# Optimization experiments

Measured on AMD Instinct MI355X. Metric: run time of the kernel, lower is better.

## Reference

```python
import jax, jax.numpy as jnp
import numpy as np

BN_EPS = 1e-5

def _bn(x, gamma, beta, relu=True):
    # training-mode BatchNorm over all dims except channel (last)
    axes = tuple(range(x.ndim - 1))
    mu = jnp.mean(x, axes, keepdims=True)
    var = jnp.var(x, axes, keepdims=True)
    y = (x - mu) / jnp.sqrt(var + BN_EPS) * gamma + beta
    return jax.nn.relu(y) if relu else y

def _l2norm(x, eps):
    # F.normalize: x / max(||x||, eps)
    n = jnp.sqrt(jnp.sum(x * x, axis=-1, keepdims=True))
    return x / jnp.maximum(n, eps)

def setup_inputs() -> dict:
    key = jax.random.key(0)
    ks = jax.random.split(key, 16)
    B, N, H, W, C = 2, 512, 16, 32, 64
    IN_DIM = 10 + C + C + 2  # 140
    MLP3 = [128, 64]
    s = 0.02
    inp = {
        "warped_xyz": jax.random.normal(ks[0], (B, N, 3), jnp.float32),
        "warped_points": jax.random.normal(ks[1], (B, N, C), jnp.float32),
        "RF3": jax.random.normal(ks[2], (B, C, H, W), jnp.float32),
        "RF3_index": jax.random.normal(ks[3], (B, 3, H, W), jnp.float32),
        "lidar_z": jax.random.uniform(ks[4], (B, N, 1), jnp.float32),
        # conv1x1 stack (mlp3)
        "W1": jax.random.normal(ks[5], (IN_DIM, MLP3[0]), jnp.float32) * s,
        "b1": jnp.zeros((MLP3[0],), jnp.float32),
        "g1": jnp.ones((MLP3[0],), jnp.float32),
        "be1": jnp.zeros((MLP3[0],), jnp.float32),
        "W2": jax.random.normal(ks[6], (MLP3[0], MLP3[1]), jnp.float32) * s,
        "b2": jnp.zeros((MLP3[1],), jnp.float32),
        "g2": jnp.ones((MLP3[1],), jnp.float32),
        "be2": jnp.zeros((MLP3[1],), jnp.float32),
        # conv1d stack (mlp4 = [feats_dim//2], then 2 logits)
        "M1w": jax.random.normal(ks[7], (MLP3[1], MLP3[1] // 2), jnp.float32) * s,
        "M1b": jnp.zeros((MLP3[1] // 2,), jnp.float32),
        "M1g": jnp.ones((MLP3[1] // 2,), jnp.float32),
        "M1be": jnp.zeros((MLP3[1] // 2,), jnp.float32),
        "M2w": jax.random.normal(ks[8], (MLP3[1] // 2, 2), jnp.float32) * s,
        "M2b": jnp.zeros((2,), jnp.float32),
    }
    return inp

def reference(warped_xyz, warped_points, RF3, RF3_index, lidar_z,
              W1, b1, g1, be1, W2, b2, g2, be2,
              M1w, M1b, M1g, M1be, M2w, M2b):
    B, N, _ = warped_xyz.shape
    _, Ci, H, W_ = RF3.shape
    M = H * W_
    RF3_bnc = RF3.transpose(0, 2, 3, 1).reshape(B, M, Ci)          # [B,M,C]
    idx_bnc = RF3_index.transpose(0, 2, 3, 1).reshape(B, M, 3)     # [B,M,3]

    src_xyz = warped_xyz[:, :, None, :]                             # [B,N,1,3]
    dst_xyz = idx_bnc[:, None, :, :]                                # [B,1,M,3]
    euc = (src_xyz - dst_xyz)[..., :2]                              # [B,N,M,2]
    euc_norm = jnp.sqrt(euc[..., 0:1] ** 2 + euc[..., 1:2] ** 2)    # [B,N,M,1]

    xyz_z = (warped_xyz * lidar_z)[:, :, None, :]                   # [B,N,1,3]
    src_pts = warped_points[:, :, None, :]                          # [B,N,1,C]
    dst_pts = RF3_bnc[:, None, :, :]                                # [B,1,M,C]

    geom = jnp.concatenate([
        jnp.broadcast_to(xyz_z, (B, N, M, 3)),
        jnp.broadcast_to(src_pts[..., :2], (B, N, M, 2)),
        jnp.broadcast_to(dst_xyz[..., :2], (B, N, M, 2)),
        euc, euc_norm], axis=-1)                                    # [B,N,M,10]
    desc = jnp.concatenate([
        jnp.broadcast_to(src_pts, (B, N, M, Ci)),
        jnp.broadcast_to(dst_pts, (B, N, M, Ci))], axis=-1)         # [B,N,M,2C]

    # cal_sim: cosine sim between lidar feats (src) and image feats (dst)
    src_n = _l2norm(warped_points, 1e-12)
    dst_n = _l2norm(RF3_bnc, 1e-12)
    cos = jnp.einsum('bnc,bmc->bnm', src_n, dst_n)                  # [B,N,M]
    s1 = cos / (jnp.max(cos, axis=2, keepdims=True) + 1e-6)         # src->dst norm
    s2 = cos / (jnp.max(cos, axis=1, keepdims=True) + 1e-10)        # dst->src norm
    sim = jnp.stack([s1, s2], axis=-1)                              # [B,N,M,2]

    feats = jnp.concatenate([geom, desc, sim], axis=-1)             # [B,N,M,140]
    feats = _bn(jnp.einsum('bnmi,io->bnmo', feats, W1) + b1, g1, be1)
    feats = _bn(jnp.einsum('bnmi,io->bnmo', feats, W2) + b2, g2, be2)

    aw = jax.nn.softmax(jnp.max(feats, axis=-1), axis=-1)           # [B,N,M]
    att = jnp.einsum('bnm,bnmc->bnc', aw, feats)                    # [B,N,C]

    att = _bn(att @ M1w + M1b, M1g, M1be)
    logits = att @ M2w + M2b                                        # [B,N,2]
    return logits
```

## Files before the change

### kernel.cpp

```cpp
#include <hip/hip_runtime.h>
#include <hip/hip_bf16.h>

#define B_ 2
#define N_ 512
#define M_ 512
#define C_ 64
#define O1 128
#define O2 64
#define O3 32
#define PBIG 524288.0f
#define P3   1024.0f

typedef short s8v __attribute__((ext_vector_type(8)));
typedef float f4v __attribute__((ext_vector_type(4)));

#define WS_SRCN 0
#define WS_DSTN 65536
#define WS_U    131072
#define WS_V    262144
#define WS_DXY  393216
#define WS_COS  395264
#define WS_RMAX 919552
#define WS_CMAX 920576
#define WS_ST1  921600
#define WS_ST2  925696
#define WS_ST3  927744
#define WS_Z    928768
#define WS_X2   961536

__device__ __forceinline__ unsigned fenc(float f){
  unsigned b = __float_as_uint(f);
  return (b & 0x80000000u) ? ~b : (b | 0x80000000u);
}
__device__ __forceinline__ float fdec(unsigned u){
  unsigned b = (u & 0x80000000u) ? (u & 0x7fffffffu) : ~u;
  return __uint_as_float(b);
}
__device__ __forceinline__ unsigned short f2bf(float f){
  unsigned u = __float_as_uint(f);
  unsigned r = (u + 0x7fffu + ((u >> 16) & 1u)) >> 16;
  return (unsigned short)r;
}
__device__ __forceinline__ float bf2f(unsigned short h){
  return __uint_as_float(((unsigned)h) << 16);
}

__global__ __launch_bounds__(128) void k1a(const float* __restrict__ wxyz,
    const float* __restrict__ wpts, const float* __restrict__ lz,
    const float* __restrict__ W1, float* __restrict__ ws){
  int blk = blockIdx.x; int b = blk >> 9, n = blk & 511; int t = threadIdx.x;
  int bn = b*N_ + n;
  __shared__ float wp[64]; __shared__ float sxyz[3]; __shared__ float slz; __shared__ float srn;
  if (t < 64) wp[t] = wpts[bn*64 + t];
  if (t >= 64 && t < 67) sxyz[t-64] = wxyz[bn*3 + (t-64)];
  if (t == 67) slz = lz[bn];
  __syncthreads();
  if (t < 64){
    float v = wp[t]*wp[t];
    v += __shfl_down(v,32); v += __shfl_down(v,16); v += __shfl_down(v,8);
    v += __shfl_down(v,4);  v += __shfl_down(v,2);  v += __shfl_down(v,1);
    if (t == 0) srn = 1.0f / fmaxf(sqrtf(v), 1e-12f);
  }
  __syncthreads();
  if (t < 64) ws[WS_SRCN + bn*64 + t] = wp[t]*srn;
  int o = t;
  float x = sxyz[0], y = sxyz[1], z = sxyz[2], l = slz;
  float acc = x*l*W1[0*O1+o] + y*l*W1[1*O1+o] + z*l*W1[2*O1+o]
            + wp[0]*W1[3*O1+o] + wp[1]*W1[4*O1+o]
            + x*W1[7*O1+o] + y*W1[8*O1+o];
  #pragma unroll 8
  for (int c = 0; c < 64; ++c) acc += wp[c]*W1[(10+c)*O1+o];
  ws[WS_U + bn*O1 + o] = acc;
}

__global__ __launch_bounds__(128) void k1b(const float* __restrict__ rf3,
    const float* __restrict__ rf3i, const float* __restrict__ W1, float* __restrict__ ws){
  int blk = blockIdx.x; int b = blk >> 9, m = blk & 511; int t = threadIdx.x;
  int bm = b*M_ + m;
  __shared__ float rf[64]; __shared__ float sdx, sdy, srn;
  if (t < 64) rf[t] = rf3[(b*64 + t)*512 + m];
  if (t == 64) sdx = rf3i[(b*3 + 0)*512 + m];
  if (t == 65) sdy = rf3i[(b*3 + 1)*512 + m];
  __syncthreads();
  if (t < 64){
    float v = rf[t]*rf[t];
    v += __shfl_down(v,32); v += __shfl_down(v,16); v += __shfl_down(v,8);
    v += __shfl_down(v,4);  v += __shfl_down(v,2);  v += __shfl_down(v,1);
    if (t == 0) srn = 1.0f / fmaxf(sqrtf(v), 1e-12f);
  }
  __syncthreads();
  if (t < 64) ws[WS_DSTN + bm*64 + t] = rf[t]*srn;
  if (t == 0){ ws[WS_DXY + bm*2+0] = sdx; ws[WS_DXY + bm*2+1] = sdy; }
  int o = t;
  float acc = sdx*(W1[5*O1+o] - W1[7*O1+o]) + sdy*(W1[6*O1+o] - W1[8*O1+o]);
  #pragma unroll 8
  for (int c = 0; c < 64; ++c) acc += rf[c]*W1[(74+c)*O1+o];
  ws[WS_V + bm*O1 + o] = acc;
}

__global__ __launch_bounds__(256) void k2(float* __restrict__ ws){
  int blk = blockIdx.x; int b = blk >> 9, n = blk & 511; int t = threadIdx.x;
  int bn = b*N_ + n;
  __shared__ __align__(16) float sn[64];
  __shared__ float dnt[64*65];
  __shared__ float part[4*64];
  if (t < 64) sn[t] = ws[WS_SRCN + bn*64 + t];
  unsigned* cmax = (unsigned*)ws + WS_CMAX;
  float lmax = -1e30f;
  for (int chunk = 0; chunk < 8; ++chunk){
    __syncthreads();
    const float4* src = (const float4*)(ws + WS_DSTN + (size_t)(b*M_ + chunk*64)*64);
    #pragma unroll
    for (int i = 0; i < 4; ++i){
      float4 v = src[t + i*256];
      int base = (t + i*256)*4; int mm = base >> 6, c = base & 63;
      float* dp = &dnt[mm*65 + c];
      dp[0]=v.x; dp[1]=v.y; dp[2]=v.z; dp[3]=v.w;
    }
    __syncthreads();
    {
      int mm = t & 63, cg = t >> 6;
      const float* dr = &dnt[mm*65 + cg*16];
      const float* sr = &sn[cg*16];
      float p = 0.f;
      #pragma unroll
      for (int k = 0; k < 16; ++k) p += sr[k]*dr[k];
      part[cg*64 + mm] = p;
    }
    __syncthreads();
    if (t < 64){
      float d = part[t] + part[64+t] + part[128+t] + part[192+t];
      int m = chunk*64 + t;
      ws[WS_COS + bn*M_ + m] = d;
      atomicMax(&cmax[b*M_ + m], fenc(d));
      lmax = fmaxf(lmax, d);
    }
  }
  if (t < 64){
    lmax = fmaxf(lmax, __shfl_xor(lmax,32)); lmax = fmaxf(lmax, __shfl_xor(lmax,16));
    lmax = fmaxf(lmax, __shfl_xor(lmax,8));  lmax = fmaxf(lmax, __shfl_xor(lmax,4));
    lmax = fmaxf(lmax, __shfl_xor(lmax,2));  lmax = fmaxf(lmax, __shfl_xor(lmax,1));
    if (t == 0) ws[WS_RMAX + bn] = lmax;
  }
}

__global__ __launch_bounds__(128) void k3(const float* __restrict__ wxyz,
    const float* __restrict__ W1, const float* __restrict__ b1, float* __restrict__ ws){
  int blk = blockIdx.x; int b = blk >> 9, n = blk & 511; int t = threadIdx.x;
  int bn = b*N_ + n;
  __shared__ float s_en[512], s_s1[512], s_s2[512];
  __shared__ float sx, sy, srm;
  if (t == 0){ sx = wxyz[bn*3+0]; sy = wxyz[bn*3+1]; srm = ws[WS_RMAX+bn]; }
  __syncthreads();
  const unsigned* cmax = (const unsigned*)ws + WS_CMAX;
  #pragma unroll
  for (int i = 0; i < 4; ++i){
    int m = t + i*128;
    float dx = ws[WS_DXY + (b*M_+m)*2+0], dy = ws[WS_DXY + (b*M_+m)*2+1];
    float ex = sx-dx, ey = sy-dy;
    s_en[m] = sqrtf(ex*ex + ey*ey);
    float cv = ws[WS_COS + bn*M_ + m];
    s_s1[m] = cv/(srm + 1e-6f);
    s_s2[m] = cv/(fdec(cmax[b*M_+m]) + 1e-10f);
  }
  __syncthreads();
  int o = t;
  float u  = ws[WS_U + bn*O1 + o] + b1[o];
  float w9 = W1[9*O1+o], wa = W1[138*O1+o], wb = W1[139*O1+o];
  float sum = 0.f, ssq = 0.f;
  const float* Vp = ws + WS_V + b*M_*O1 + o;
  #pragma unroll 8
  for (int m = 0; m < 512; ++m){
    float xv = u + Vp[m*O1] + s_en[m]*w9 + s_s1[m]*wa + s_s2[m]*wb;
    sum += xv; ssq += xv*xv;
  }
  int rep = blk & 15;
  atomicAdd(&ws[WS_ST1 + rep*256 + o], sum);
  atomicAdd(&ws[WS_ST1 + rep*256 + 128 + o], ssq);
}

#define HROW 136
__global__ __launch_bounds__(256) void k4(const float* __restrict__ wxyz,
    const float* __restrict__ W1, const float* __restrict__ b1,
    const float* __restrict__ g1, const float* __restrict__ be1,
    const float* __restrict__ W2, float* __restrict__ ws){
  int blk = blockIdx.x;
  int b = blk >> 11; int rem = blk & 2047; int n = rem >> 2; int mc = rem & 3;
  int t = threadIdx.x; int bn = b*N_ + n; int m0 = mc*128;
  __shared__ unsigned short hA[128*HROW];
  __shared__ unsigned short wB[64*HROW];
  __shared__ float s_en[128], s_s1[128], s_s2[128];
  __shared__ float sP0[128], sA1[128], sW9[128], sWa[128], sWb[128];
  __shared__ float ls[64], lq[64];
  __shared__ float sx, sy, srm;
  if (t == 128) sx = wxyz[bn*3+0];
  if (t == 129) sy = wxyz[bn*3+1];
  if (t == 130) srm = ws[WS_RMAX+bn];
  if (t < 64){ ls[t] = 0.f; lq[t] = 0.f; }
  if (t < 128){
    int o = t; float s = 0.f, q = 0.f;
    #pragma unroll
    for (int r = 0; r < 16; ++r){ s += ws[WS_ST1 + r*256 + o]; q += ws[WS_ST1 + r*256 + 128 + o]; }
    float mu = s/PBIG; float var = q/PBIG - mu*mu;
    float istd = rsqrtf(var + 1e-5f);
    float A1 = g1[o]*istd; float C1 = be1[o] - mu*A1;
    float u = ws[WS_U + bn*O1 + o] + b1[o];
    sP0[o] = u*A1 + C1; sA1[o] = A1;
    sW9[o] = W1[9*O1+o]*A1; sWa[o] = W1[138*O1+o]*A1; sWb[o] = W1[139*O1+o]*A1;
  }
  for (int idx = t; idx < 8192; idx += 256){
    int o = idx >> 6, c = idx & 63;
    wB[c*HROW + o] = f2bf(W2[idx]);
  }
  __syncthreads();
  if (t < 128){
    int m = m0 + t;
    float dx = ws[WS_DXY + (b*M_+m)*2+0], dy = ws[WS_DXY + (b*M_+m)*2+1];
    float ex = sx-dx, ey = sy-dy;
    s_en[t] = sqrtf(ex*ex + ey*ey);
    float cv = ws[WS_COS + bn*M_ + m];
    s_s1[t] = cv/(srm + 1e-6f);
    s_s2[t] = cv/(fdec(((const unsigned*)ws)[WS_CMAX + b*M_+m]) + 1e-10f);
  }
  __syncthreads();
  {
    int lane = t & 63, g = t >> 6;
    const float* Vb = ws + WS_V + (size_t)(b*M_ + m0)*O1;
    int o0 = 2*lane;
    #pragma unroll 8
    for (int i = 0; i < 32; ++i){
      int ml = g + 4*i;
      float en = s_en[ml], s1 = s_s1[ml], s2 = s_s2[ml];
      float2 v = *(const float2*)(Vb + ml*O1 + o0);
      float h0 = fmaxf(sP0[o0]   + v.x*sA1[o0]   + en*sW9[o0]   + s1*sWa[o0]   + s2*sWb[o0],   0.f);
      float h1 = fmaxf(sP0[o0+1] + v.y*sA1[o0+1] + en*sW9[o0+1] + s1*sWa[o0+1] + s2*sWb[o0+1], 0.f);
      unsigned pack = (unsigned)f2bf(h0) | ((unsigned)f2bf(h1) << 16);
      *(unsigned*)&hA[ml*HROW + o0] = pack;
    }
  }
  __syncthreads();
  int lane = t & 63, w = t >> 6;
  int l16 = lane & 15, quad = lane >> 4;
  f4v acc[2][4];
  #pragma unroll
  for (int i = 0; i < 2; ++i)
    #pragma unroll
    for (int j = 0; j < 4; ++j) acc[i][j] = (f4v){0.f,0.f,0.f,0.f};
  int ar0 = (w*32 + l16)*HROW, ar1 = (w*32 + 16 + l16)*HROW;
  #pragma unroll
  for (int k0 = 0; k0 < 128; k0 += 32){
    int ko = k0 + quad*8;
    s8v a0 = *(const s8v*)&hA[ar0 + ko];
    s8v a1 = *(const s8v*)&hA[ar1 + ko];
    #pragma unroll
    for (int ct = 0; ct < 4; ++ct){
      s8v bb = *(const s8v*)&wB[(ct*16 + l16)*HROW + ko];
      acc[0][ct] = __builtin_amdgcn_mfma_f32_16x16x32_bf16(a0, bb, acc[0][ct], 0,0,0);
      acc[1][ct] = __builtin_amdgcn_mfma_f32_16x16x32_bf16(a1, bb, acc[1][ct], 0,0,0);
    }
  }
  unsigned short* x2p = (unsigned short*)(ws + WS_X2);
  size_t xbase = (size_t)bn*M_*O2;
  #pragma unroll
  for (int ct = 0; ct < 4; ++ct){
    int c = ct*16 + l16;
    float s = 0.f, q = 0.f;
    #pragma unroll
    for (int mt = 0; mt < 2; ++mt){
      #pragma unroll
      for (int r = 0; r < 4; ++r){
        float v = acc[mt][ct][r];
        int m = m0 + w*32 + mt*16 + quad*4 + r;
        x2p[xbase + (size_t)m*O2 + c] = f2bf(v);
        s += v; q += v*v;
      }
    }
    s += __shfl_xor(s,16); s += __shfl_xor(s,32);
    q += __shfl_xor(q,16); q += __shfl_xor(q,32);
    if (quad == 0){ atomicAdd(&ls[c], s); atomicAdd(&lq[c], q); }
  }
  __syncthreads();
  int rep = blk & 15;
  if (t < 64) atomicAdd(&ws[WS_ST2 + rep*128 + t], ls[t]);
  else if (t < 128) atomicAdd(&ws[WS_ST2 + rep*128 + t], lq[t-64]);
}

__global__ __launch_bounds__(256) void k5(const float* __restrict__ g2,
    const float* __restrict__ be2, const float* __restrict__ M1w,
    const float* __restrict__ M1b, float* __restrict__ ws){
  int blk = blockIdx.x; int b = blk >> 9, n = blk & 511; int t = threadIdx.x;
  int bn = b*N_ + n;
  __shared__ float sa2[64], sc2[64];
  __shared__ float s_mx[512];
  __shared__ float s_aw[512];
  __shared__ float red[256];
  __shared__ float part[32*64];
  __shared__ float s_att[64];
  __shared__ float sgmax, sinvS;
  if (t < 64){
    float s = 0.f, q = 0.f;
    #pragma unroll
    for (int r = 0; r < 16; ++r){ s += ws[WS_ST2 + r*128 + t]; q += ws[WS_ST2 + r*128 + 64 + t]; }
    float mu = s/PBIG, var = q/PBIG - mu*mu;
    float istd = rsqrtf(var + 1e-5f);
    float A2 = g2[t]*istd;
    sa2[t] = A2; sc2[t] = be2[t] - mu*A2;
  }
  __syncthreads();
  int j8 = t & 7, r32 = t >> 3;
  int c0 = j8*8;
  float a2r[8], c2r[8];
  #pragma unroll
  for (int j = 0; j < 8; ++j){ a2r[j] = sa2[c0+j]; c2r[j] = sc2[c0+j]; }
  const unsigned short* xp = (const unsigned short*)(ws + WS_X2) + (size_t)bn*M_*O2;
  s8v xv[16];
  #pragma unroll
  for (int s = 0; s < 16; ++s)
    xv[s] = *(const s8v*)(xp + (size_t)(s*32 + r32)*64 + c0);
  #pragma unroll
  for (int s = 0; s < 16; ++s){
    float mx = 0.f;
    #pragma unroll
    for (int j = 0; j < 8; ++j){
      float x = bf2f((unsigned short)xv[s][j]);
      float y = fmaxf(a2r[j]*x + c2r[j], 0.f);
      mx = fmaxf(mx, y);
    }
    mx = fmaxf(mx, __shfl_xor(mx,1));
    mx = fmaxf(mx, __shfl_xor(mx,2));
    mx = fmaxf(mx, __shfl_xor(mx,4));
    if (j8 == 0) s_mx[s*32 + r32] = mx;
  }
  __syncthreads();
  red[t] = fmaxf(s_mx[t], s_mx[t+256]);
  __syncthreads();
  for (int s = 128; s > 0; s >>= 1){ if (t < s) red[t] = fmaxf(red[t], red[t+s]); __syncthreads(); }
  if (t == 0) sgmax = red[0];
  __syncthreads();
  float e0 = expf(s_mx[t] - sgmax), e1 = expf(s_mx[t+256] - sgmax);
  s_aw[t] = e0; s_aw[t+256] = e1;
  red[t] = e0 + e1;
  __syncthreads();
  for (int s = 128; s > 0; s >>= 1){ if (t < s) red[t] += red[t+s]; __syncthreads(); }
  if (t == 0) sinvS = 1.0f / red[0];
  __syncthreads();
  float acc[8];
  #pragma unroll
  for (int j = 0; j < 8; ++j) acc[j] = 0.f;
  #pragma unroll
  for (int s = 0; s < 16; ++s){
    float aw = s_aw[s*32 + r32];
    #pragma unroll
    for (int j = 0; j < 8; ++j){
      float x = bf2f((unsigned short)xv[s][j]);
      float y = fmaxf(a2r[j]*x + c2r[j], 0.f);
      acc[j] += aw*y;
    }
  }
  #pragma unroll
  for (int j = 0; j < 8; ++j) part[r32*64 + c0 + j] = acc[j];
  __syncthreads();
  if (t < 64){
    float a = 0.f;
    #pragma unroll 8
    for (int r = 0; r < 32; ++r) a += part[r*64 + t];
    s_att[t] = a * sinvS;
  }
  __syncthreads();
  if (t < 32){
    float z = M1b[t];
    #pragma unroll 8
    for (int c = 0; c < 64; ++c) z += s_att[c]*M1w[c*32 + t];
    ws[WS_Z + bn*32 + t] = z;
    int rep = blk & 15;
    atomicAdd(&ws[WS_ST3 + rep*64 + t], z);
    atomicAdd(&ws[WS_ST3 + rep*64 + 32 + t], z*z);
  }
}

__global__ __launch_bounds__(256) void k6(const float* __restrict__ M1g,
    const float* __restrict__ M1be, const float* __restrict__ M2w,
    const float* __restrict__ M2b, const float* __restrict__ ws, float* __restrict__ out){
  int t = threadIdx.x; int s = blockIdx.x*256 + t;
  __shared__ float sa3[32], sc3[32];
  if (t < 32){
    float su = 0.f, q = 0.f;
    #pragma unroll
    for (int r = 0; r < 16; ++r){ su += ws[WS_ST3 + r*64 + t]; q += ws[WS_ST3 + r*64 + 32 + t]; }
    float mu = su/P3, var = q/P3 - mu*mu;
    float istd = rsqrtf(var + 1e-5f);
    float A3 = M1g[t]*istd;
    sa3[t] = A3; sc3[t] = M1be[t] - mu*A3;
  }
  __syncthreads();
  float a0 = M2b[0], a1 = M2b[1];
  #pragma unroll
  for (int j = 0; j < 32; ++j){
    float y = fmaxf(ws[WS_Z + s*32 + j]*sa3[j] + sc3[j], 0.f);
    a0 += y*M2w[j*2+0]; a1 += y*M2w[j*2+1];
  }
  out[s*2+0] = a0; out[s*2+1] = a1;
}

extern "C" void kernel_launch(void* const* d_in, const int* in_sizes, int n_in,
                              void* d_out, int out_size, void* d_ws, size_t ws_size,
                              hipStream_t stream){
  const float* wxyz = (const float*)d_in[0];
  const float* wpts = (const float*)d_in[1];
  const float* rf3  = (const float*)d_in[2];
  const float* rf3i = (const float*)d_in[3];
  const float* lz   = (const float*)d_in[4];
  const float* W1   = (const float*)d_in[5];
  const float* b1   = (const float*)d_in[6];
  const float* g1   = (const float*)d_in[7];
  const float* be1  = (const float*)d_in[8];
  const float* W2   = (const float*)d_in[9];
  const float* g2   = (const float*)d_in[11];
  const float* be2  = (const float*)d_in[12];
  const float* M1w  = (const float*)d_in[13];
  const float* M1b  = (const float*)d_in[14];
  const float* M1g  = (const float*)d_in[15];
  const float* M1be = (const float*)d_in[16];
  const float* M2w  = (const float*)d_in[17];
  const float* M2b  = (const float*)d_in[18];
  float* ws  = (float*)d_ws;
  float* out = (float*)d_out;
  hipMemsetAsync(ws + WS_CMAX, 0, (1024 + 4096 + 2048 + 1024)*sizeof(float), stream);
  k1a<<<1024,128,0,stream>>>(wxyz, wpts, lz, W1, ws);
  k1b<<<1024,128,0,stream>>>(rf3, rf3i, W1, ws);
  k2 <<<1024,256,0,stream>>>(ws);
  k3 <<<1024,128,0,stream>>>(wxyz, W1, b1, ws);
  k4 <<<4096,256,0,stream>>>(wxyz, W1, b1, g1, be1, W2, ws);
  k5 <<<1024,256,0,stream>>>(g2, be2, M1w, M1b, ws);
  k6 <<<4,256,0,stream>>>(M1g, M1be, M2w, M2b, ws, out);
}
```

Measured before the change: 247.6 us.

## Precompute BN1 folding and W2 fragments once; build MFMA A operands in registers

A new k3b kernel folds the BN1 scale and shift into per-point P0, pre-scaled V and W9/Wa/Wb vectors, and writes W2 as bf16 in MFMA-fragment order to workspace. k4 no longer recomputes the BN statistics or re-converts W2 in each of its 4096 blocks. It also builds the bf16 A operands directly in registers with truncating packs instead of staging them through shared memory, and it swaps operand order to get coalesced packed stores. k3 is split over 256 threads with half the m range each. Costs are an extra kernel launch plus a pass over V, and bf16 truncation in place of round-to-nearest, which changes numerics slightly.

```diff
diff --git a/kernel.cpp b/kernel.cpp
--- a/kernel.cpp
+++ b/kernel.cpp
@@ -16,6 +16,7 @@
 
 #define WS_SRCN 0
 #define WS_DSTN 65536
+#define WS_P0   0
 #define WS_U    131072
 #define WS_V    262144
 #define WS_DXY  393216
@@ -26,6 +27,8 @@
 #define WS_ST2  925696
 #define WS_ST3  927744
 #define WS_Z    928768
+#define WS_W2F  928768
+#define WS_W9S  932864
 #define WS_X2   961536
 
 __device__ __forceinline__ unsigned fenc(float f){
@@ -43,6 +46,14 @@
 }
 __device__ __forceinline__ float bf2f(unsigned short h){
   return __uint_as_float(((unsigned)h) << 16);
+}
+__device__ __forceinline__ unsigned pk_trunc(float lo, float hi){
+  return __builtin_amdgcn_perm(__float_as_uint(hi), __float_as_uint(lo), 0x07060302u);
+}
+__device__ __forceinline__ f4v relu4(f4v z){
+  z[0] = fmaxf(z[0], 0.f); z[1] = fmaxf(z[1], 0.f);
+  z[2] = fmaxf(z[2], 0.f); z[3] = fmaxf(z[3], 0.f);
+  return z;
 }
 
 __global__ __launch_bounds__(128) void k1a(const float* __restrict__ wxyz,
@@ -144,7 +155,7 @@
   }
 }
 
-__global__ __launch_bounds__(128) void k3(const float* __restrict__ wxyz,
+__global__ __launch_bounds__(256) void k3(const float* __restrict__ wxyz,
     const float* __restrict__ W1, const float* __restrict__ b1, float* __restrict__ ws){
   int blk = blockIdx.x; int b = blk >> 9, n = blk & 511; int t = threadIdx.x;
   int bn = b*N_ + n;
@@ -154,8 +165,8 @@
   __syncthreads();
   const unsigned* cmax = (const unsigned*)ws + WS_CMAX;
   #pragma unroll
-  for (int i = 0; i < 4; ++i){
-    int m = t + i*128;
+  for (int i = 0; i < 2; ++i){
+    int m = t + i*256;
     float dx = ws[WS_DXY + (b*M_+m)*2+0], dy = ws[WS_DXY + (b*M_+m)*2+1];
     float ex = sx-dx, ey = sy-dy;
     s_en[m] = sqrtf(ex*ex + ey*ey);
@@ -164,13 +175,14 @@
     s_s2[m] = cv/(fdec(cmax[b*M_+m]) + 1e-10f);
   }
   __syncthreads();
-  int o = t;
+  int o = t & 127, mh = t >> 7;
   float u  = ws[WS_U + bn*O1 + o] + b1[o];
   float w9 = W1[9*O1+o], wa = W1[138*O1+o], wb = W1[139*O1+o];
   float sum = 0.f, ssq = 0.f;
   const float* Vp = ws + WS_V + b*M_*O1 + o;
+  int mBeg = mh*256, mEnd = mBeg + 256;
   #pragma unroll 8
-  for (int m = 0; m < 512; ++m){
+  for (int m = mBeg; m < mEnd; ++m){
     float xv = u + Vp[m*O1] + s_en[m]*w9 + s_s1[m]*wa + s_s2[m]*wb;
     sum += xv; ssq += xv*xv;
   }
@@ -179,38 +191,60 @@
   atomicAdd(&ws[WS_ST1 + rep*256 + 128 + o], ssq);
 }
 
-#define HROW 136
-__global__ __launch_bounds__(256) void k4(const float* __restrict__ wxyz,
-    const float* __restrict__ W1, const float* __restrict__ b1,
-    const float* __restrict__ g1, const float* __restrict__ be1,
-    const float* __restrict__ W2, float* __restrict__ ws){
+__global__ __launch_bounds__(128) void k3b(const float* __restrict__ W1,
+    const float* __restrict__ b1, const float* __restrict__ g1,
+    const float* __restrict__ be1, const float* __restrict__ W2, float* __restrict__ ws){
+  int blk = blockIdx.x; int t = threadIdx.x;
+  int o = t;
+  float s = 0.f, q = 0.f;
+  #pragma unroll
+  for (int r = 0; r < 16; ++r){ s += ws[WS_ST1 + r*256 + o]; q += ws[WS_ST1 + r*256 + 128 + o]; }
+  float mu = s/PBIG, var = q/PBIG - mu*mu;
+  float istd = rsqrtf(var + 1e-5f);
+  float A1 = g1[o]*istd, C1 = be1[o] - mu*A1;
+  if (blk < 1024){
+    int bn = blk;
+    ws[WS_P0 + bn*O1 + o] = (ws[WS_U + bn*O1 + o] + b1[o])*A1 + C1;
+  } else if (blk < 1040){
+    int r0 = (blk - 1024)*64;
+    for (int r = 0; r < 64; ++r)
+      ws[WS_V + (size_t)(r0 + r)*O1 + o] *= A1;
+  } else {
+    ws[WS_W9S + o]       = W1[9*O1+o]*A1;
+    ws[WS_W9S + 128 + o] = W1[138*O1+o]*A1;
+    ws[WS_W9S + 256 + o] = W1[139*O1+o]*A1;
+    unsigned short* wf = (unsigned short*)(ws + WS_W2F);
+    for (int i = t; i < 8192; i += 128){
+      int j = i & 7, ll = (i >> 3) & 63, ct = (i >> 9) & 3, k0q = i >> 11;
+      int oo = k0q*32 + (ll >> 4)*8 + j, c = ct*16 + (ll & 15);
+      wf[i] = f2bf(W2[oo*O2 + c]);
+    }
+  }
+}
+
+__global__ __launch_bounds__(256, 4) void k4(const float* __restrict__ wxyz,
+    float* __restrict__ ws){
   int blk = blockIdx.x;
   int b = blk >> 11; int rem = blk & 2047; int n = rem >> 2; int mc = rem & 3;
   int t = threadIdx.x; int bn = b*N_ + n; int m0 = mc*128;
-  __shared__ unsigned short hA[128*HROW];
-  __shared__ unsigned short wB[64*HROW];
+  __shared__ __align__(16) unsigned short wBf[8192];
+  __shared__ __align__(16) float p0s[128], w9s[128], was[128], wbs[128];
   __shared__ float s_en[128], s_s1[128], s_s2[128];
-  __shared__ float sP0[128], sA1[128], sW9[128], sWa[128], sWb[128];
   __shared__ float ls[64], lq[64];
   __shared__ float sx, sy, srm;
-  if (t == 128) sx = wxyz[bn*3+0];
-  if (t == 129) sy = wxyz[bn*3+1];
-  if (t == 130) srm = ws[WS_RMAX+bn];
+  if (t == 0){ sx = wxyz[bn*3+0]; sy = wxyz[bn*3+1]; srm = ws[WS_RMAX+bn]; }
   if (t < 64){ ls[t] = 0.f; lq[t] = 0.f; }
+  {
+    const s8v* g = (const s8v*)(ws + WS_W2F);
+    s8v* l = (s8v*)wBf;
+    #pragma unroll
+    for (int c2 = 0; c2 < 4; ++c2) l[c2*256 + t] = g[c2*256 + t];
+  }
   if (t < 128){
-    int o = t; float s = 0.f, q = 0.f;
-    #pragma unroll
-    for (int r = 0; r < 16; ++r){ s += ws[WS_ST1 + r*256 + o]; q += ws[WS_ST1 + r*256 + 128 + o]; }
-    float mu = s/PBIG; float var = q/PBIG - mu*mu;
-    float istd = rsqrtf(var + 1e-5f);
-    float A1 = g1[o]*istd; float C1 = be1[o] - mu*A1;
-    float u = ws[WS_U + bn*O1 + o] + b1[o];
-    sP0[o] = u*A1 + C1; sA1[o] = A1;
-    sW9[o] = W1[9*O1+o]*A1; sWa[o] = W1[138*O1+o]*A1; sWb[o] = W1[139*O1+o]*A1;
-  }
-  for (int idx = t; idx < 8192; idx += 256){
-    int o = idx >> 6, c = idx & 63;
-    wB[c*HROW + o] = f2bf(W2[idx]);
+    p0s[t] = ws[WS_P0 + bn*O1 + t];
+    w9s[t] = ws[WS_W9S + t];
+    was[t] = ws[WS_W9S + 128 + t];
+    wbs[t] = ws[WS_W9S + 256 + t];
   }
   __syncthreads();
   if (t < 128){
@@ -223,61 +257,66 @@
     s_s2[t] = cv/(fdec(((const unsigned*)ws)[WS_CMAX + b*M_+m]) + 1e-10f);
   }
   __syncthreads();
-  {
-    int lane = t & 63, g = t >> 6;
-    const float* Vb = ws + WS_V + (size_t)(b*M_ + m0)*O1;
-    int o0 = 2*lane;
-    #pragma unroll 8
-    for (int i = 0; i < 32; ++i){
-      int ml = g + 4*i;
-      float en = s_en[ml], s1 = s_s1[ml], s2 = s_s2[ml];
-      float2 v = *(const float2*)(Vb + ml*O1 + o0);
-      float h0 = fmaxf(sP0[o0]   + v.x*sA1[o0]   + en*sW9[o0]   + s1*sWa[o0]   + s2*sWb[o0],   0.f);
-      float h1 = fmaxf(sP0[o0+1] + v.y*sA1[o0+1] + en*sW9[o0+1] + s1*sWa[o0+1] + s2*sWb[o0+1], 0.f);
-      unsigned pack = (unsigned)f2bf(h0) | ((unsigned)f2bf(h1) << 16);
-      *(unsigned*)&hA[ml*HROW + o0] = pack;
-    }
-  }
-  __syncthreads();
-  int lane = t & 63, w = t >> 6;
-  int l16 = lane & 15, quad = lane >> 4;
+  int ll = t & 63, w = t >> 6, l16 = ll & 15, quad = ll >> 4;
+  int mb = m0 + w*32;
+  float en0 = s_en[w*32 + l16],     s10 = s_s1[w*32 + l16],     s20 = s_s2[w*32 + l16];
+  float en1 = s_en[w*32 + 16 + l16], s11 = s_s1[w*32 + 16 + l16], s21 = s_s2[w*32 + 16 + l16];
   f4v acc[2][4];
   #pragma unroll
   for (int i = 0; i < 2; ++i)
     #pragma unroll
     for (int j = 0; j < 4; ++j) acc[i][j] = (f4v){0.f,0.f,0.f,0.f};
-  int ar0 = (w*32 + l16)*HROW, ar1 = (w*32 + 16 + l16)*HROW;
-  #pragma unroll
-  for (int k0 = 0; k0 < 128; k0 += 32){
-    int ko = k0 + quad*8;
-    s8v a0 = *(const s8v*)&hA[ar0 + ko];
-    s8v a1 = *(const s8v*)&hA[ar1 + ko];
+  const float* Vb = ws + WS_V + (size_t)(b*M_ + mb)*O1;
+  union U8 { s8v v; unsigned u[4]; };
+  #pragma unroll
+  for (int k0q = 0; k0q < 4; ++k0q){
+    int ko = k0q*32 + quad*8;
+    f4v p0a = *(const f4v*)&p0s[ko], p0b = *(const f4v*)&p0s[ko+4];
+    f4v w9a = *(const f4v*)&w9s[ko], w9b = *(const f4v*)&w9s[ko+4];
+    f4v waa = *(const f4v*)&was[ko], wab = *(const f4v*)&was[ko+4];
+    f4v wba = *(const f4v*)&wbs[ko], wbb = *(const f4v*)&wbs[ko+4];
+    s8v af[2];
+    #pragma unroll
+    for (int mt = 0; mt < 2; ++mt){
+      const float* vp = Vb + (size_t)(mt*16 + l16)*O1 + ko;
+      f4v va = *(const f4v*)vp, vb = *(const f4v*)(vp+4);
+      float en = mt ? en1 : en0, s1 = mt ? s11 : s10, s2 = mt ? s21 : s20;
+      f4v za = relu4(p0a + va + en*w9a + s1*waa + s2*wba);
+      f4v zb = relu4(p0b + vb + en*w9b + s1*wab + s2*wbb);
+      U8 u8;
+      u8.u[0] = pk_trunc(za[0], za[1]);
+      u8.u[1] = pk_trunc(za[2], za[3]);
+      u8.u[2] = pk_trunc(zb[0], zb[1]);
+      u8.u[3] = pk_trunc(zb[2], zb[3]);
+      af[mt] = u8.v;
+    }
     #pragma unroll
     for (int ct = 0; ct < 4; ++ct){
-      s8v bb = *(const s8v*)&wB[(ct*16 + l16)*HROW + ko];
-      acc[0][ct] = __builtin_amdgcn_mfma_f32_16x16x32_bf16(a0, bb, acc[0][ct], 0,0,0);
-      acc[1][ct] = __builtin_amdgcn_mfma_f32_16x16x32_bf16(a1, bb, acc[1][ct], 0,0,0);
-    }
-  }
-  unsigned short* x2p = (unsigned short*)(ws + WS_X2);
-  size_t xbase = (size_t)bn*M_*O2;
+      s8v bb = *(const s8v*)&wBf[((k0q*4 + ct)*64 + ll)*8];
+      acc[0][ct] = __builtin_amdgcn_mfma_f32_16x16x32_bf16(bb, af[0], acc[0][ct], 0,0,0);
+      acc[1][ct] = __builtin_amdgcn_mfma_f32_16x16x32_bf16(bb, af[1], acc[1][ct], 0,0,0);
+    }
+  }
+  unsigned short* x2p = (unsigned short*)(ws + WS_X2) + (size_t)bn*M_*O2;
   #pragma unroll
   for (int ct = 0; ct < 4; ++ct){
-    int c = ct*16 + l16;
-    float s = 0.f, q = 0.f;
+    int c0 = ct*16 + quad*4;
     #pragma unroll
     for (int mt = 0; mt < 2; ++mt){
-      #pragma unroll
-      for (int r = 0; r < 4; ++r){
-        float v = acc[mt][ct][r];
-        int m = m0 + w*32 + mt*16 + quad*4 + r;
-        x2p[xbase + (size_t)m*O2 + c] = f2bf(v);
-        s += v; q += v*v;
-      }
-    }
-    s += __shfl_xor(s,16); s += __shfl_xor(s,32);
-    q += __shfl_xor(q,16); q += __shfl_xor(q,32);
-    if (quad == 0){ atomicAdd(&ls[c], s); atomicAdd(&lq[c], q); }
+      int m = mb + mt*16 + l16;
+      uint2 uv;
+      uv.x = (unsigned)f2bf(acc[mt][ct][0]) | ((unsigned)f2bf(acc[mt][ct][1]) << 16);
+      uv.y = (unsigned)f2bf(acc[mt][ct][2]) | ((unsigned)f2bf(acc[mt][ct][3]) << 16);
+      *(uint2*)(x2p + (size_t)m*O2 + c0) = uv;
+    }
+    #pragma unroll
+    for (int r = 0; r < 4; ++r){
+      float s = acc[0][ct][r] + acc[1][ct][r];
+      float q = acc[0][ct][r]*acc[0][ct][r] + acc[1][ct][r]*acc[1][ct][r];
+      s += __shfl_xor(s,1); s += __shfl_xor(s,2); s += __shfl_xor(s,4); s += __shfl_xor(s,8);
+      q += __shfl_xor(q,1); q += __shfl_xor(q,2); q += __shfl_xor(q,4); q += __shfl_xor(q,8);
+      if (l16 == 0){ atomicAdd(&ls[c0 + r], s); atomicAdd(&lq[c0 + r], q); }
+    }
   }
   __syncthreads();
   int rep = blk & 15;
@@ -429,8 +468,9 @@
   k1a<<<1024,128,0,stream>>>(wxyz, wpts, lz, W1, ws);
   k1b<<<1024,128,0,stream>>>(rf3, rf3i, W1, ws);
   k2 <<<1024,256,0,stream>>>(ws);
-  k3 <<<1024,128,0,stream>>>(wxyz, W1, b1, ws);
-  k4 <<<4096,256,0,stream>>>(wxyz, W1, b1, g1, be1, W2, ws);
+  k3 <<<1024,256,0,stream>>>(wxyz, W1, b1, ws);
+  k3b<<<1041,128,0,stream>>>(W1, b1, g1, be1, W2, ws);
+  k4 <<<4096,256,0,stream>>>(wxyz, ws);
   k5 <<<1024,256,0,stream>>>(g2, be2, M1w, M1b, ws);
   k6 <<<4,256,0,stream>>>(M1g, M1be, M2w, M2b, ws, out);
 }
```

New measurement: 239.3 us. -3.4%, faster.
